# Optimization experiments

Measured on AMD Instinct MI355X. Metric: run time of the kernel, lower is better.

Reference implementation:

```python
import jax, jax.numpy as jnp
import numpy as np

D_MODEL = 1024
N_HEADS = 16
DEPTH = D_MODEL // N_HEADS
NEG_INF = -1.0e9


def setup_inputs() -> dict:
    key = jax.random.key(0)
    ks = jax.random.split(key, 11)
    B, S = 2, 2048
    xk = jax.random.normal(ks[0], (B, S, D_MODEL), jnp.float32)
    xq = jax.random.normal(ks[1], (B, S, D_MODEL), jnp.float32)
    xv = jax.random.normal(ks[2], (B, S, D_MODEL), jnp.float32)
    sc = 1.0 / np.sqrt(D_MODEL)
    wq = jax.random.normal(ks[3], (D_MODEL, D_MODEL), jnp.float32) * sc
    wk = jax.random.normal(ks[4], (D_MODEL, D_MODEL), jnp.float32) * sc
    wv = jax.random.normal(ks[5], (D_MODEL, D_MODEL), jnp.float32) * sc
    wo = jax.random.normal(ks[6], (D_MODEL, D_MODEL), jnp.float32) * sc
    bq = jnp.zeros((D_MODEL,), jnp.float32)
    bk = jnp.zeros((D_MODEL,), jnp.float32)
    bv = jnp.zeros((D_MODEL,), jnp.float32)
    bo = jnp.zeros((D_MODEL,), jnp.float32)
    return {"xk": xk, "xq": xq, "xv": xv, "wq": wq, "bq": bq, "wk": wk,
            "bk": bk, "wv": wv, "bv": bv, "wo": wo, "bo": bo}


def _split_heads(t):
    # [B, S, D] -> [B, H, S, depth]
    B, S, _ = t.shape
    return t.reshape(B, S, N_HEADS, DEPTH).transpose(0, 2, 1, 3)


def reference(xk, xq, xv, wq, bq, wk, bk, wv, bv, wo, bo):
    B, Sq, _ = xq.shape
    Sk = xk.shape[1]
    q = _split_heads(xq @ wq + bq)  # [B,H,Sq,d]
    k = _split_heads(xk @ wk + bk)  # [B,H,Sk,d]
    v = _split_heads(xv @ wv + bv)  # [B,H,Sk,d]
    logits = jnp.einsum('bhqd,bhkd->bhqk', q, k) / jnp.sqrt(
        jnp.asarray(DEPTH, q.dtype))
    # additive causal mask: (1 - lower_triangular) * -1e9
    causal = (1.0 - jnp.tril(jnp.ones((Sq, Sk), logits.dtype))) * NEG_INF
    logits = logits + causal[None, None, :, :]
    attn = jax.nn.softmax(logits, axis=-1)
    out = jnp.einsum('bhqk,bhkd->bhqd', attn, v)
    out = out.transpose(0, 2, 1, 3).reshape(B, Sq, D_MODEL)
    return out @ wo + bo
```

## Files before the change

### kernel.cpp

```cpp
#include <hip/hip_runtime.h>

typedef unsigned short u16;
typedef unsigned int u32;
typedef u16 u16x8 __attribute__((ext_vector_type(8)));
typedef u32 u32x4 __attribute__((ext_vector_type(4)));
typedef __bf16 bf16x8 __attribute__((ext_vector_type(8)));
typedef float f32x4 __attribute__((ext_vector_type(4)));
typedef float f32x16 __attribute__((ext_vector_type(16)));

#define DM 1024
#define SEQ 2048
#define BATCH 2
#define MROWS 4096

__device__ __forceinline__ u16 f2bf(float f) {
  unsigned int x = __builtin_bit_cast(unsigned int, f);
  x += 0x7fffu + ((x >> 16) & 1u);
  return (u16)(x >> 16);
}

__device__ __forceinline__ void gld16(const void* g, void* l) {
  __builtin_amdgcn_global_load_lds(
      (const __attribute__((address_space(1))) void*)g,
      (__attribute__((address_space(3))) void*)l, 16, 0, 0);
}

__device__ __forceinline__ u32 cvtpk_bf16(float lo, float hi) {
  u32 r;
  asm("v_cvt_pk_bf16_f32 %0, %1, %2" : "=v"(r) : "v"(lo), "v"(hi));
  return r;
}
__device__ __forceinline__ void pl32swap(u32& x, u32& y) {
  asm volatile("v_permlane32_swap_b32 %0, %1" : "+v"(x), "+v"(y));
}

struct TrArgs { const float* in[4]; u16* out[4]; };

__global__ __launch_bounds__(256) void transpose_w4(TrArgs a) {
  const float* __restrict__ in = a.in[blockIdx.z];
  u16* __restrict__ out = a.out[blockIdx.z];
  __shared__ u16 T[64][72];
  int r0 = blockIdx.y * 64, c0 = blockIdx.x * 64;
  int t = threadIdx.x;
  int r = t >> 3, cg = (t & 7) * 8;
#pragma unroll
  for (int p = 0; p < 2; p++) {
    const float* src = in + (size_t)(r0 + r + p * 32) * DM + c0 + cg;
    f32x4 x0 = *(const f32x4*)src;
    f32x4 x1 = *(const f32x4*)(src + 4);
    u16x8 v;
#pragma unroll
    for (int j = 0; j < 4; j++) { v[j] = f2bf(x0[j]); v[4 + j] = f2bf(x1[j]); }
    *(u16x8*)(&T[r + p * 32][cg]) = v;
  }
  __syncthreads();
#pragma unroll
  for (int p = 0; p < 2; p++) {
    int orow = r + p * 32;
    u16x8 v;
#pragma unroll
    for (int j = 0; j < 8; j++) v[j] = T[cg + j][orow];
    *(u16x8*)(out + (size_t)(c0 + orow) * DM + r0 + cg) = v;
  }
}

struct CastArgs { const float* in[3]; u16* out[3]; };

__global__ __launch_bounds__(256) void cast_x(CastArgs a) {
  const float* __restrict__ in = a.in[blockIdx.y];
  u16* __restrict__ out = a.out[blockIdx.y];
  size_t e = ((size_t)blockIdx.x * 256 + threadIdx.x) * 8;
  f32x4 a0 = *(const f32x4*)(in + e);
  f32x4 a1 = *(const f32x4*)(in + e + 4);
  u16x8 v;
#pragma unroll
  for (int j = 0; j < 4; j++) { v[j] = f2bf(a0[j]); v[4 + j] = f2bf(a1[j]); }
  *(u16x8*)(out + e) = v;
}

struct GemmArgs { const void* A[3]; const u16* WT[3]; const float* bias[3]; void* C[3]; };

template <int MT, int NT, bool AF32, bool OF32>
__global__ __launch_bounds__(256) void gemmT(GemmArgs g) {
  __shared__ __align__(16) u16 As[MT * 32 * 32];
  __shared__ __align__(16) u16 Bs[NT * 32 * 32];
  const int z = blockIdx.z;
  const u16* __restrict__ WT = g.WT[z];
  const int tid = threadIdx.x;
  const int lane = tid & 63, wave = tid >> 6;
  const int fr = lane & 15, kq = lane >> 4;
  const int mq = (wave >> 1) * (MT * 16), nq = (wave & 1) * (NT * 16);
  const int m0 = blockIdx.y * (MT * 32), n0 = blockIdx.x * (NT * 32);
  const int srow = tid >> 2;
  const int scA = ((tid & 3) ^ ((srow >> 1) & 3)) * 8;
  const int fco = ((kq ^ ((fr >> 1) & 3)) * 8);
  f32x4 acc[MT][NT] = {};

  for (int kk = 0; kk < DM; kk += 32) {
    __syncthreads();
    if constexpr (AF32) {
      const float* A = (const float*)g.A[z];
#pragma unroll
      for (int i = 0; i < MT / 2; i++) {
        const float* s0 = A + (size_t)(m0 + i * 64 + srow) * DM + kk + scA;
        f32x4 a0 = *(const f32x4*)s0, a1 = *(const f32x4*)(s0 + 4);
        u16x8 v;
#pragma unroll
        for (int j = 0; j < 4; j++) { v[j] = f2bf(a0[j]); v[4 + j] = f2bf(a1[j]); }
        *(u16x8*)(As + (i * 256 + tid) * 8) = v;
      }
    } else {
      const u16* A = (const u16*)g.A[z];
#pragma unroll
      for (int i = 0; i < MT / 2; i++)
        gld16(A + (size_t)(m0 + i * 64 + srow) * DM + kk + scA,
              As + (i * 256 + tid) * 8);
    }
#pragma unroll
    for (int i = 0; i < NT / 2; i++)
      gld16(WT + (size_t)(n0 + i * 64 + srow) * DM + kk + scA,
            Bs + (i * 256 + tid) * 8);
    __syncthreads();
    bf16x8 af[MT], bfr[NT];
#pragma unroll
    for (int mt = 0; mt < MT; mt++)
      af[mt] = __builtin_bit_cast(
          bf16x8, *(const u16x8*)(As + (mq + mt * 16 + fr) * 32 + fco));
#pragma unroll
    for (int nt = 0; nt < NT; nt++)
      bfr[nt] = __builtin_bit_cast(
          bf16x8, *(const u16x8*)(Bs + (nq + nt * 16 + fr) * 32 + fco));
#pragma unroll
    for (int mt = 0; mt < MT; mt++)
#pragma unroll
      for (int nt = 0; nt < NT; nt++)
        acc[mt][nt] =
            __builtin_amdgcn_mfma_f32_16x16x32_bf16(af[mt], bfr[nt], acc[mt][nt], 0, 0, 0);
  }
  const float* __restrict__ bias = g.bias[z];
#pragma unroll
  for (int nt = 0; nt < NT; nt++) {
    int col = n0 + nq + nt * 16 + fr;
    float bb = bias[col];
#pragma unroll
    for (int mt = 0; mt < MT; mt++)
#pragma unroll
      for (int r = 0; r < 4; r++) {
        int row = m0 + mq + mt * 16 + kq * 4 + r;
        float val = acc[mt][nt][r] + bb;
        if constexpr (OF32)
          ((float*)g.C[z])[(size_t)row * DM + col] = val;
        else
          ((u16*)g.C[z])[(size_t)row * DM + col] = f2bf(val);
      }
  }
}

#define KS 72
__global__ __launch_bounds__(512, 4) void attn3(u16* __restrict__ Q,
                                                const u16* __restrict__ K,
                                                const u16* __restrict__ V) {
  __shared__ __align__(16) u16 Ksh[2][64 * 64];
  __shared__ __align__(16) u16 Vt[2][64 * KS];
  __shared__ float cmb[128][49];
  const int tid = threadIdx.x, wave = tid >> 6, lane = tid & 63;
  const int ql = lane & 31, hi = lane >> 5;
  const int grp = wave >> 2, w4 = wave & 3;
  const int pair = w4 >> 1, w01 = w4 & 1;
  const int b = blockIdx.x >> 4, h = blockIdx.x & 15;
  const int by = blockIdx.y;
  const int y = (by < 8) ? by : 23 - by;
  const int qtA = 31 - y;
  const int qt = grp ? y : qtA;
  const float C1 = 0.125f * 1.44269504f;

  const int krow = tid >> 3;
  const int kcs = ((tid & 7) ^ (krow & 7)) * 8;
  const u16* Kg = K + (size_t)(b * SEQ + krow) * DM + h * 64 + kcs;
  const u16* Vg = V + (size_t)(b * SEQ + lane) * DM + h * 64 + wave * 8;

  int xsl[4];
#pragma unroll
  for (int f = 0; f < 4; f++) xsl[f] = ((2 * f + hi) ^ (ql & 7)) * 8;

  bf16x8 qf[4];
  {
    size_t qr = (size_t)(b * SEQ + qt * 64 + w01 * 32 + ql) * DM + h * 64;
#pragma unroll
    for (int f = 0; f < 4; f++)
      qf[f] = __builtin_bit_cast(bf16x8,
                                 *(const u16x8*)(Q + qr + f * 16 + hi * 8));
  }

  u16x8 onesu;
#pragma unroll
  for (int j = 0; j < 8; j++) onesu[j] = 0x3F80;
  const bf16x8 vones = __builtin_bit_cast(bf16x8, onesu);

  f32x16 ov0 = {}, ov1 = {}, ovl = {};

  gld16(Kg, Ksh[0] + tid * 8);
  {
    u16x8 v0 = *(const u16x8*)(Vg);
#pragma unroll
    for (int j = 0; j < 8; j++) Vt[0][(wave * 8 + j) * KS + lane] = v0[j];
  }
  __syncthreads();

  int cur = 0;
  for (int t = 0; t <= qtA; t++) {
    const int nb = cur ^ 1;
    u16x8 nv0;
    const bool pf = (t < qtA);
    if (pf) {
      size_t ro = (size_t)(t + 1) * 64 * DM;
      gld16(Kg + ro, Ksh[nb] + tid * 8);
      nv0 = *(const u16x8*)(Vg + ro);
    }
    if (grp == 1 && pair == 0 && t == qt + 1) {
      const float* src = cmb[w01 * 64 + lane];
      float o0[16], o1[16], rl[16];
#pragma unroll
      for (int r = 0; r < 16; r++) {
        o0[r] = ov0[r] + src[r];
        o1[r] = ov1[r] + src[16 + r];
        rl[r] = 1.0f / (ovl[r] + src[32 + r]);
      }
#pragma unroll
      for (int r = 0; r < 16; r++) {
        int row = qt * 64 + w01 * 32 + (r & 3) + 8 * (r >> 2) + 4 * hi;
        size_t base = (size_t)(b * SEQ + row) * DM + h * 64 + ql;
        Q[base] = f2bf(o0[r] * rl[r]);
        Q[base + 32] = f2bf(o1[r] * rl[r]);
      }
    }
    if (t <= qt) {
      const u16* Kc = Ksh[cur];
      f32x16 s = {};
#pragma unroll
      for (int f = 0; f < 4; f++) {
        bf16x8 a0 = __builtin_bit_cast(
            bf16x8, *(const u16x8*)(Kc + (pair * 32 + ql) * 64 + xsl[f]));
        s = __builtin_amdgcn_mfma_f32_32x32x16_bf16(a0, qf[f], s, 0, 0, 0);
      }
      if (t == qt) {
        int qg = qt * 64 + w01 * 32 + ql;
        int kb = t * 64 + pair * 32 + 4 * hi;
#pragma unroll
        for (int r = 0; r < 16; r++) {
          int key = kb + (r & 3) + 8 * (r >> 2);
          if (key > qg) s[r] = -1e30f;
        }
      }
      const u16* Vc = Vt[cur];
      {
        float p[16];
#pragma unroll
        for (int r = 0; r < 16; r++)
          p[r] = __builtin_amdgcn_exp2f(s[r] * C1);
#pragma unroll
        for (int ss = 0; ss < 2; ss++) {
          u32 w0 = cvtpk_bf16(p[ss * 8 + 0], p[ss * 8 + 1]);
          u32 w1 = cvtpk_bf16(p[ss * 8 + 2], p[ss * 8 + 3]);
          u32 w2 = cvtpk_bf16(p[ss * 8 + 4], p[ss * 8 + 5]);
          u32 w3 = cvtpk_bf16(p[ss * 8 + 6], p[ss * 8 + 7]);
          pl32swap(w0, w2);
          pl32swap(w1, w3);
          u32x4 paw = {w0, w1, w2, w3};
          bf16x8 pa = __builtin_bit_cast(bf16x8, paw);
          const int kb2 = pair * 32 + ss * 16 + hi * 8;
          bf16x8 vb0 = __builtin_bit_cast(
              bf16x8, *(const u16x8*)(Vc + ql * KS + kb2));
          ov0 = __builtin_amdgcn_mfma_f32_32x32x16_bf16(pa, vb0, ov0, 0, 0, 0);
          bf16x8 vb1 = __builtin_bit_cast(
              bf16x8, *(const u16x8*)(Vc + (32 + ql) * KS + kb2));
          ov1 = __builtin_amdgcn_mfma_f32_32x32x16_bf16(pa, vb1, ov1, 0, 0, 0);
          ovl = __builtin_amdgcn_mfma_f32_32x32x16_bf16(pa, vones, ovl, 0, 0, 0);
        }
      }
      if (grp == 1 && pair == 1 && t == qt) {
        float* dst = cmb[w01 * 64 + lane];
#pragma unroll
        for (int r = 0; r < 16; r++) {
          dst[r] = ov0[r];
          dst[16 + r] = ov1[r];
          dst[32 + r] = ovl[r];
        }
      }
    }
    if (pf) {
#pragma unroll
      for (int j = 0; j < 8; j++) Vt[nb][(wave * 8 + j) * KS + lane] = nv0[j];
    }
    __syncthreads();
    cur = nb;
  }
  if (grp == 0 && pair == 1) {
    float* dst = cmb[w01 * 64 + lane];
#pragma unroll
    for (int r = 0; r < 16; r++) {
      dst[r] = ov0[r];
      dst[16 + r] = ov1[r];
      dst[32 + r] = ovl[r];
    }
  }
  __syncthreads();
  if (grp == 0 && pair == 0) {
    const float* src = cmb[w01 * 64 + lane];
    float rl[16];
#pragma unroll
    for (int r = 0; r < 16; r++) {
      ov0[r] += src[r];
      ov1[r] += src[16 + r];
      rl[r] = 1.0f / (ovl[r] + src[32 + r]);
    }
#pragma unroll
    for (int r = 0; r < 16; r++) {
      int row = qt * 64 + w01 * 32 + (r & 3) + 8 * (r >> 2) + 4 * hi;
      size_t base = (size_t)(b * SEQ + row) * DM + h * 64 + ql;
      Q[base] = f2bf(ov0[r] * rl[r]);
      Q[base + 32] = f2bf(ov1[r] * rl[r]);
    }
  }
}

extern "C" void kernel_launch(void* const* d_in, const int* in_sizes, int n_in,
                              void* d_out, int out_size, void* d_ws,
                              size_t ws_size, hipStream_t stream) {
  const float* xk = (const float*)d_in[0];
  const float* xq = (const float*)d_in[1];
  const float* xv = (const float*)d_in[2];
  const float* wq = (const float*)d_in[3];
  const float* bq = (const float*)d_in[4];
  const float* wk = (const float*)d_in[5];
  const float* bk = (const float*)d_in[6];
  const float* wv = (const float*)d_in[7];
  const float* bv = (const float*)d_in[8];
  const float* wo = (const float*)d_in[9];
  const float* bo = (const float*)d_in[10];

  u16* Qb = (u16*)d_ws;
  u16* Kb = Qb + (size_t)MROWS * DM;
  u16* Vb = Kb + (size_t)MROWS * DM;
  u16* WTq = Vb + (size_t)MROWS * DM;
  u16* WTk = WTq + (size_t)DM * DM;
  u16* WTv = WTk + (size_t)DM * DM;
  u16* WTo = WTv + (size_t)DM * DM;
  u16* Xq = WTo + (size_t)DM * DM;
  u16* Xk = Xq + (size_t)MROWS * DM;
  u16* Xv = Xk + (size_t)MROWS * DM;
  const bool cast_path =
      ws_size >= ((size_t)(3 * 8 + 4 * 2 + 3 * 8)) * 1024 * 1024;

  dim3 blk(256);

  TrArgs tr;
  tr.in[0] = wq; tr.in[1] = wk; tr.in[2] = wv; tr.in[3] = wo;
  tr.out[0] = WTq; tr.out[1] = WTk; tr.out[2] = WTv; tr.out[3] = WTo;
  transpose_w4<<<dim3(16, 16, 4), blk, 0, stream>>>(tr);

  GemmArgs gq;
  gq.WT[0] = WTq; gq.WT[1] = WTk; gq.WT[2] = WTv;
  gq.bias[0] = bq; gq.bias[1] = bk; gq.bias[2] = bv;
  gq.C[0] = Qb; gq.C[1] = Kb; gq.C[2] = Vb;
  if (cast_path) {
    CastArgs ca;
    ca.in[0] = xq; ca.in[1] = xk; ca.in[2] = xv;
    ca.out[0] = Xq; ca.out[1] = Xk; ca.out[2] = Xv;
    cast_x<<<dim3(MROWS * DM / 2048, 3), blk, 0, stream>>>(ca);
    gq.A[0] = Xq; gq.A[1] = Xk; gq.A[2] = Xv;
    gemmT<4, 4, false, false>
        <<<dim3(DM / 128, MROWS / 128, 3), blk, 0, stream>>>(gq);
  } else {
    gq.A[0] = xq; gq.A[1] = xk; gq.A[2] = xv;
    gemmT<4, 4, true, false>
        <<<dim3(DM / 128, MROWS / 128, 3), blk, 0, stream>>>(gq);
  }

  attn3<<<dim3(BATCH * 16, 16), dim3(512), 0, stream>>>(Qb, Kb, Vb);

  GemmArgs go;
  go.A[0] = Qb;  go.WT[0] = WTo; go.bias[0] = bo; go.C[0] = d_out;
  go.A[1] = Qb;  go.WT[1] = WTo; go.bias[1] = bo; go.C[1] = d_out;
  go.A[2] = Qb;  go.WT[2] = WTo; go.bias[2] = bo; go.C[2] = d_out;
  gemmT<2, 4, false, true>
      <<<dim3(DM / 128, MROWS / 64, 1), blk, 0, stream>>>(go);
}
```

Before: 264.0 us.

## Double GEMM K-tile depth to 64, enlarge output GEMM tile, relax attn occupancy bound

The GEMM main loop now stages 64-wide K slices per iteration instead of 32, using a new XOR swizzle over 8 chunks. This halves the number of barrier pairs and makes each global load wider per row. The output projection switches from 64x128 to 128x128 tiles, which gives more reuse per block but half as many blocks. The attention kernel drops its min-blocks-per-CU hint, letting the compiler use more registers at the possible cost of occupancy.

```diff
diff --git a/kernel.cpp b/kernel.cpp
--- a/kernel.cpp
+++ b/kernel.cpp
@@ -82,8 +82,8 @@
 
 template <int MT, int NT, bool AF32, bool OF32>
 __global__ __launch_bounds__(256) void gemmT(GemmArgs g) {
-  __shared__ __align__(16) u16 As[MT * 32 * 32];
-  __shared__ __align__(16) u16 Bs[NT * 32 * 32];
+  __shared__ __align__(16) u16 As[MT * 32 * 64];
+  __shared__ __align__(16) u16 Bs[NT * 32 * 64];
   const int z = blockIdx.z;
   const u16* __restrict__ WT = g.WT[z];
   const int tid = threadIdx.x;
@@ -91,18 +91,19 @@
   const int fr = lane & 15, kq = lane >> 4;
   const int mq = (wave >> 1) * (MT * 16), nq = (wave & 1) * (NT * 16);
   const int m0 = blockIdx.y * (MT * 32), n0 = blockIdx.x * (NT * 32);
-  const int srow = tid >> 2;
-  const int scA = ((tid & 3) ^ ((srow >> 1) & 3)) * 8;
-  const int fco = ((kq ^ ((fr >> 1) & 3)) * 8);
+  const int srow = tid >> 3;
+  const int scol = ((tid & 7) ^ (srow & 7)) * 8;
+  const int x0 = (kq ^ (fr & 7)) * 8;
+  const int x1 = ((4 + kq) ^ (fr & 7)) * 8;
   f32x4 acc[MT][NT] = {};
 
-  for (int kk = 0; kk < DM; kk += 32) {
+  for (int kk = 0; kk < DM; kk += 64) {
     __syncthreads();
     if constexpr (AF32) {
       const float* A = (const float*)g.A[z];
 #pragma unroll
-      for (int i = 0; i < MT / 2; i++) {
-        const float* s0 = A + (size_t)(m0 + i * 64 + srow) * DM + kk + scA;
+      for (int i = 0; i < MT; i++) {
+        const float* s0 = A + (size_t)(m0 + i * 32 + srow) * DM + kk + scol;
         f32x4 a0 = *(const f32x4*)s0, a1 = *(const f32x4*)(s0 + 4);
         u16x8 v;
 #pragma unroll
@@ -112,30 +113,34 @@
     } else {
       const u16* A = (const u16*)g.A[z];
 #pragma unroll
-      for (int i = 0; i < MT / 2; i++)
-        gld16(A + (size_t)(m0 + i * 64 + srow) * DM + kk + scA,
+      for (int i = 0; i < MT; i++)
+        gld16(A + (size_t)(m0 + i * 32 + srow) * DM + kk + scol,
               As + (i * 256 + tid) * 8);
     }
 #pragma unroll
-    for (int i = 0; i < NT / 2; i++)
-      gld16(WT + (size_t)(n0 + i * 64 + srow) * DM + kk + scA,
+    for (int i = 0; i < NT; i++)
+      gld16(WT + (size_t)(n0 + i * 32 + srow) * DM + kk + scol,
             Bs + (i * 256 + tid) * 8);
     __syncthreads();
-    bf16x8 af[MT], bfr[NT];
-#pragma unroll
-    for (int mt = 0; mt < MT; mt++)
-      af[mt] = __builtin_bit_cast(
-          bf16x8, *(const u16x8*)(As + (mq + mt * 16 + fr) * 32 + fco));
-#pragma unroll
-    for (int nt = 0; nt < NT; nt++)
-      bfr[nt] = __builtin_bit_cast(
-          bf16x8, *(const u16x8*)(Bs + (nq + nt * 16 + fr) * 32 + fco));
-#pragma unroll
-    for (int mt = 0; mt < MT; mt++)
+#pragma unroll
+    for (int hf = 0; hf < 2; hf++) {
+      const int xo = hf ? x1 : x0;
+      bf16x8 af[MT], bfr[NT];
+#pragma unroll
+      for (int mt = 0; mt < MT; mt++)
+        af[mt] = __builtin_bit_cast(
+            bf16x8, *(const u16x8*)(As + (mq + mt * 16 + fr) * 64 + xo));
 #pragma unroll
       for (int nt = 0; nt < NT; nt++)
-        acc[mt][nt] =
-            __builtin_amdgcn_mfma_f32_16x16x32_bf16(af[mt], bfr[nt], acc[mt][nt], 0, 0, 0);
+        bfr[nt] = __builtin_bit_cast(
+            bf16x8, *(const u16x8*)(Bs + (nq + nt * 16 + fr) * 64 + xo));
+#pragma unroll
+      for (int mt = 0; mt < MT; mt++)
+#pragma unroll
+        for (int nt = 0; nt < NT; nt++)
+          acc[mt][nt] = __builtin_amdgcn_mfma_f32_16x16x32_bf16(
+              af[mt], bfr[nt], acc[mt][nt], 0, 0, 0);
+    }
   }
   const float* __restrict__ bias = g.bias[z];
 #pragma unroll
@@ -157,9 +162,9 @@
 }
 
 #define KS 72
-__global__ __launch_bounds__(512, 4) void attn3(u16* __restrict__ Q,
-                                                const u16* __restrict__ K,
-                                                const u16* __restrict__ V) {
+__global__ __launch_bounds__(512) void attn3(u16* __restrict__ Q,
+                                             const u16* __restrict__ K,
+                                             const u16* __restrict__ V) {
   __shared__ __align__(16) u16 Ksh[2][64 * 64];
   __shared__ __align__(16) u16 Vt[2][64 * KS];
   __shared__ float cmb[128][49];
@@ -383,6 +388,6 @@
   go.A[0] = Qb;  go.WT[0] = WTo; go.bias[0] = bo; go.C[0] = d_out;
   go.A[1] = Qb;  go.WT[1] = WTo; go.bias[1] = bo; go.C[1] = d_out;
   go.A[2] = Qb;  go.WT[2] = WTo; go.bias[2] = bo; go.C[2] = d_out;
-  gemmT<2, 4, false, true>
-      <<<dim3(DM / 128, MROWS / 64, 1), blk, 0, stream>>>(go);
-}
+  gemmT<4, 4, false, true>
+      <<<dim3(DM / 128, MROWS / 128, 1), blk, 0, stream>>>(go);
+}
```

New measurement: 251.9 us. -4.6%, faster.
